# Kernel optimization log

Measured on AMD Instinct MI355X. Metric: run time of the kernel, lower is better.

The kernel has to match this reference:

```python
import jax, jax.numpy as jnp
import numpy as np

B, S, H = 16, 2048, 768
MAX_NUM = 400     # max relation pairs per sample (ragged, masked)
LABELS = 97
MID = 768


def setup_inputs() -> dict:
    key = jax.random.key(0)
    k1, k2, k3, k4, k5 = jax.random.split(key, 5)
    outs = jax.random.normal(k1, (B, S, H), dtype=jnp.float32)
    rels = jax.random.randint(k2, (B, MAX_NUM), 0, LABELS)
    start = jnp.ones((B,), dtype=jnp.int32)                     # markers start at pos 1
    num = jax.random.randint(k3, (B,), 1, MAX_NUM + 1)          # ragged counts in [1, MAX_NUM]
    rels_pos = jnp.stack([start, num], axis=1)                  # [B, 2]
    W1 = jax.random.normal(k4, (2 * H, MID), dtype=jnp.float32) * (1.0 / np.sqrt(2 * H))
    b1 = jnp.zeros((MID,), dtype=jnp.float32)
    W2 = jax.random.normal(k5, (MID, LABELS), dtype=jnp.float32) * (1.0 / np.sqrt(MID))
    b2 = jnp.zeros((LABELS,), dtype=jnp.float32)
    return {"outs": outs, "rels": rels, "rels_pos": rels_pos,
            "W1": W1, "b1": b1, "W2": W2, "b2": b2}


def reference(outs, rels, rels_pos, W1, b1, W2, b2):
    # outs: [B, S, H] encoder hidden states; rels_pos[:, 0]=start, [:, 1]=num (ragged)
    start = rels_pos[:, 0]          # [B]
    num = rels_pos[:, 1]            # [B]
    i = jnp.arange(MAX_NUM)         # [N]
    mask = i[None, :] < num[:, None]                 # [B, N] valid-pair mask
    pos1 = start[:, None] + 4 * i[None, :]           # head marker positions
    pos2 = pos1 + 2                                  # tail marker positions
    pos1 = jnp.clip(pos1, 0, S - 1)
    pos2 = jnp.clip(pos2, 0, S - 1)
    v1 = jnp.take_along_axis(outs, pos1[:, :, None], axis=1)   # [B, N, H]
    v2 = jnp.take_along_axis(outs, pos2[:, :, None], axis=1)   # [B, N, H]
    marker_vec = jnp.concatenate([v1, v2], axis=-1)             # [B, N, 2H]
    h = jax.nn.relu(jnp.einsum('bnd,dm->bnm', marker_vec, W1) + b1)
    logits = jnp.einsum('bnm,ml->bnl', h, W2) + b2              # [B, N, L]
    logp = jax.nn.log_softmax(logits, axis=-1)
    nll = -jnp.take_along_axis(logp, rels[:, :, None], axis=-1)[..., 0]  # [B, N]
    maskf = mask.astype(logits.dtype)
    loss = jnp.sum(nll * maskf) / jnp.sum(maskf)                # mean CE over valid pairs
    pred = jnp.where(mask, jnp.argmax(logits, axis=-1), -1)     # [B, N], -1 = padding
    label_vec = jnp.where(mask, rels, -1)
    return loss, pred, label_vec
```

## Files before the change

kernel.cpp:

```cpp
#include <hip/hip_runtime.h>
#include <hip/hip_bf16.h>
#include <math.h>

#define BB   16
#define SS   2048
#define HH   768
#define MAXN 400
#define LBL  97
#define MIDD 768
#define KTOT 1536

#define K2_XTILES 25
#define W1S_JOBS  (192 * 768)
#define K1_RT     7
#define K1_GROUPS (K1_RT * BB)
#define K1_BLOCKS (K1_GROUPS * 6)

typedef __attribute__((ext_vector_type(8)))  __bf16 bf16x8;
typedef __attribute__((ext_vector_type(16))) float  f32x16;

__global__ __launch_bounds__(256)
void k0_split(const float* __restrict__ W1, ushort* __restrict__ hi,
              ushort* __restrict__ lo)
{
    const int job = blockIdx.x * 256 + threadIdx.x;
    if (job >= W1S_JOBS) return;
    const int g   = job / 768;
    const int col = job - g * 768;
    bf16x8 hv, lv;
    #pragma unroll
    for (int j = 0; j < 8; ++j) {
        const float f = W1[(size_t)(g * 8 + j) * MIDD + col];
        const __bf16 hb = (__bf16)f;
        hv[j] = hb;
        lv[j] = (__bf16)(f - (float)hb);
    }
    ((bf16x8*)hi)[job] = hv;
    ((bf16x8*)lo)[job] = lv;
}

__global__ __launch_bounds__(256, 2)
void k1_gemm1(const float* __restrict__ outs, const int* __restrict__ rels_pos,
              const ushort* __restrict__ w1hi, const ushort* __restrict__ w1lo,
              const float* __restrict__ b1, float* __restrict__ h)
{
    const int gid = blockIdx.x;
    const int idx = gid >> 3;
    const int g   = (gid & 7) + 8 * (idx / 6);
    const int m   = idx % 6;
    const int rt  = g % K1_RT;
    const int b   = g / K1_RT;
    const int n0  = m * 128;
    const int i0  = rt * 64;

    const int num = rels_pos[2 * b + 1];
    if (i0 >= num) return;
    const int start = rels_pos[2 * b + 0];

    __shared__ __bf16 Ah[4][64][8];
    __shared__ __bf16 Al[4][64][8];
    __shared__ __bf16 Bh[4][128][8];
    __shared__ __bf16 Bl[4][128][8];

    const int tid = threadIdx.x;

    const int srow = tid & 63;
    const int sg   = tid >> 6;
    const int irow = i0 + srow;
    int p1 = start + 4 * irow;     p1 = min(max(p1, 0), SS - 1);
    int p2 = start + 4 * irow + 2; p2 = min(max(p2, 0), SS - 1);
    const float* arow1 = outs + (size_t)(b * SS + p1) * HH;
    const float* arow2 = outs + (size_t)(b * SS + p2) * HH;

    const int bc  = tid & 127;
    const int bg1 = tid >> 7;
    const int bg2 = 2 + (tid >> 7);
    const bf16x8* WH = (const bf16x8*)w1hi;
    const bf16x8* WL = (const bf16x8*)w1lo;

    const int lane = tid & 63;
    const int wid  = tid >> 6;
    const int wr   = wid >> 1;
    const int wc   = wid & 1;
    const int l31  = lane & 31;
    const int lhi  = lane >> 5;

    f32x16 acc[2];
    #pragma unroll
    for (int n = 0; n < 2; ++n)
        #pragma unroll
        for (int j = 0; j < 16; ++j) acc[n][j] = 0.f;

    float4 aU0, aV0, aU1, aV1;
    bf16x8 pB00, pB01, pB02, pB03, pB10, pB11, pB12, pB13;

    {
        const int k = sg * 8;
        const float* s = arow1 + k;
        aU0 = *(const float4*)(s);
        aV0 = *(const float4*)(s + 4);
        const size_t i1 = (size_t)bg1 * 768 + n0 + bc;
        const size_t i2 = (size_t)bg2 * 768 + n0 + bc;
        pB00 = WH[i1]; pB01 = WL[i1]; pB02 = WH[i2]; pB03 = WL[i2];
    }
    {
        const int k = 32 + sg * 8;
        const float* s = arow1 + k;
        aU1 = *(const float4*)(s);
        aV1 = *(const float4*)(s + 4);
        const size_t base = (size_t)(32 >> 3) * 768 + n0 + bc;
        const size_t i1 = base + (size_t)bg1 * 768;
        const size_t i2 = base + (size_t)bg2 * 768;
        pB10 = WH[i1]; pB11 = WL[i1]; pB12 = WH[i2]; pB13 = WL[i2];
    }

    #define K1_STAGE(AU, AV, P0, P1_, P2_, P3_)                               \
        {                                                                     \
            const float fa[8] = {AU.x, AU.y, AU.z, AU.w,                      \
                                 AV.x, AV.y, AV.z, AV.w};                     \
            bf16x8 ah, al;                                                    \
            _Pragma("unroll")                                                 \
            for (int j = 0; j < 8; ++j) {                                     \
                const __bf16 hb = (__bf16)fa[j];                              \
                ah[j] = hb;                                                   \
                al[j] = (__bf16)(fa[j] - (float)hb);                          \
            }                                                                 \
            *(bf16x8*)&Ah[sg][srow][0] = ah;                                  \
            *(bf16x8*)&Al[sg][srow][0] = al;                                  \
            *(bf16x8*)&Bh[bg1][bc][0]  = P0;                                  \
            *(bf16x8*)&Bl[bg1][bc][0]  = P1_;                                 \
            *(bf16x8*)&Bh[bg2][bc][0]  = P2_;                                 \
            *(bf16x8*)&Bl[bg2][bc][0]  = P3_;                                 \
        }

    #define K1_LOAD(AU, AV, P0, P1_, P2_, P3_, KT)                            \
        {                                                                     \
            const int k0 = (KT) * 32;                                         \
            const int k  = k0 + sg * 8;                                       \
            const float* s = (k < HH) ? (arow1 + k) : (arow2 + (k - HH));     \
            AU = *(const float4*)(s);                                         \
            AV = *(const float4*)(s + 4);                                     \
            const size_t base = (size_t)(k0 >> 3) * 768 + n0 + bc;            \
            const size_t i1 = base + (size_t)bg1 * 768;                       \
            const size_t i2 = base + (size_t)bg2 * 768;                       \
            P0 = WH[i1]; P1_ = WL[i1]; P2_ = WH[i2]; P3_ = WL[i2];            \
        }

    #define K1_MFMA()                                                         \
        _Pragma("unroll")                                                     \
        for (int s = 0; s < 2; ++s) {                                         \
            const int kg   = 2 * s + lhi;                                     \
            const int arow = wr * 32 + l31;                                   \
            const bf16x8 xh = *(const bf16x8*)&Ah[kg][arow][0];               \
            const bf16x8 xl = *(const bf16x8*)&Al[kg][arow][0];               \
            _Pragma("unroll")                                                 \
            for (int n = 0; n < 2; ++n) {                                     \
                const int bcol = wc * 64 + n * 32 + l31;                      \
                const bf16x8 yh = *(const bf16x8*)&Bh[kg][bcol][0];           \
                const bf16x8 yl = *(const bf16x8*)&Bl[kg][bcol][0];           \
                acc[n] = __builtin_amdgcn_mfma_f32_32x32x16_bf16(xh, yh, acc[n], 0, 0, 0); \
                acc[n] = __builtin_amdgcn_mfma_f32_32x32x16_bf16(xh, yl, acc[n], 0, 0, 0); \
                acc[n] = __builtin_amdgcn_mfma_f32_32x32x16_bf16(xl, yh, acc[n], 0, 0, 0); \
            }                                                                 \
        }

    for (int kt = 0; kt < KTOT / 32; kt += 2) {
        K1_STAGE(aU0, aV0, pB00, pB01, pB02, pB03);
        __syncthreads();
        if (kt + 2 < KTOT / 32) K1_LOAD(aU0, aV0, pB00, pB01, pB02, pB03, kt + 2);
        K1_MFMA();
        __syncthreads();
        K1_STAGE(aU1, aV1, pB10, pB11, pB12, pB13);
        __syncthreads();
        if (kt + 3 < KTOT / 32) K1_LOAD(aU1, aV1, pB10, pB11, pB12, pB13, kt + 3);
        K1_MFMA();
        __syncthreads();
    }
    #undef K1_STAGE
    #undef K1_LOAD
    #undef K1_MFMA

    #pragma unroll
    for (int n = 0; n < 2; ++n) {
        const int colg = n0 + wc * 64 + n * 32 + l31;
        const float bv = b1[colg];
        #pragma unroll
        for (int j = 0; j < 16; ++j) {
            const int row = (j & 3) + 8 * (j >> 2) + 4 * lhi;
            const int i = i0 + wr * 32 + row;
            if (i < MAXN)
                h[((size_t)b * MAXN + i) * MIDD + colg] = fmaxf(acc[n][j] + bv, 0.f);
        }
    }
}

__global__ __launch_bounds__(256, 2)
void k2_head(const float* __restrict__ h, const int* __restrict__ rels,
             const int* __restrict__ rels_pos,
             const float* __restrict__ W2, const float* __restrict__ b2,
             float* __restrict__ out, float* __restrict__ partials)
{
    const int b   = blockIdx.y;
    const int i0  = blockIdx.x * 16;
    const int num = rels_pos[2 * b + 1];
    const int tid = threadIdx.x;
    const int blk = blockIdx.y * gridDim.x + blockIdx.x;

    if (tid < 16) {
        const int i = i0 + tid;
        if (i < MAXN && i >= num) {
            out[1 + b * MAXN + i] = -1.0f;
            out[1 + BB * MAXN + b * MAXN + i] = -1.0f;
        }
    }
    if (i0 >= num) { if (tid == 0) partials[blk] = 0.f; return; }

    __shared__ __align__(16) float hs[MIDD][16];
    __shared__ float wave_nll[4];

    {
        const int row = tid & 15;
        const int kc0 = (tid >> 4) * 4;
        const int hrow_i = min(i0 + row, MAXN - 1);
        const float* hrow = h + ((size_t)b * MAXN + hrow_i) * MIDD;
        #pragma unroll
        for (int j = 0; j < 12; ++j) {
            const int k = kc0 + j * 64;
            const float4 v = *(const float4*)(hrow + k);
            hs[k + 0][row] = v.x;
            hs[k + 1][row] = v.y;
            hs[k + 2][row] = v.z;
            hs[k + 3][row] = v.w;
        }
    }
    __syncthreads();

    const int lane = tid & 63;
    const int wv   = tid >> 6;
    const int c    = lane;
    const bool has2 = (lane + 64) < LBL;
    const int c2   = has2 ? (lane + 64) : (LBL - 1);

    float acc0[4], acc1[4];
    #pragma unroll
    for (int r = 0; r < 4; ++r) { acc0[r] = 0.f; acc1[r] = 0.f; }

    float wA[8], wB[8], nAr[8], nBr[8];
    #pragma unroll
    for (int j = 0; j < 8; ++j) {
        wA[j] = W2[(size_t)j * LBL + c];
        wB[j] = W2[(size_t)j * LBL + c2];
    }
    for (int kbase = 0; kbase < MIDD; kbase += 8) {
        const bool more = (kbase + 8) < MIDD;
        if (more) {
            #pragma unroll
            for (int j = 0; j < 8; ++j) {
                nAr[j] = W2[(size_t)(kbase + 8 + j) * LBL + c];
                nBr[j] = W2[(size_t)(kbase + 8 + j) * LBL + c2];
            }
        }
        #pragma unroll
        for (int j = 0; j < 8; ++j) {
            const float4 hv = *(const float4*)&hs[kbase + j][wv * 4];
            acc0[0] += hv.x * wA[j]; acc0[1] += hv.y * wA[j];
            acc0[2] += hv.z * wA[j]; acc0[3] += hv.w * wA[j];
            acc1[0] += hv.x * wB[j]; acc1[1] += hv.y * wB[j];
            acc1[2] += hv.z * wB[j]; acc1[3] += hv.w * wB[j];
        }
        if (more) {
            #pragma unroll
            for (int j = 0; j < 8; ++j) { wA[j] = nAr[j]; wB[j] = nBr[j]; }
        }
    }
    const float bc  = b2[c];
    const float bc2 = b2[c2];
    #pragma unroll
    for (int r = 0; r < 4; ++r) { acc0[r] += bc; acc1[r] += bc2; }

    float nll_acc = 0.f;
    #pragma unroll
    for (int r = 0; r < 4; ++r) {
        const int i = i0 + wv * 4 + r;
        if (i >= num || i >= MAXN) continue;
        const float v1 = acc0[r];
        const float v2 = has2 ? acc1[r] : -INFINITY;
        float bv = v1; int bi = c;
        if (v2 > v1) { bv = v2; bi = lane + 64; }
        #pragma unroll
        for (int off = 32; off > 0; off >>= 1) {
            const float ov = __shfl_xor(bv, off);
            const int   oi = __shfl_xor(bi, off);
            if (ov > bv || (ov == bv && oi < bi)) { bv = ov; bi = oi; }
        }
        float se = expf(v1 - bv) + (has2 ? expf(v2 - bv) : 0.f);
        #pragma unroll
        for (int off = 32; off > 0; off >>= 1) se += __shfl_xor(se, off);
        const int lbl = rels[b * MAXN + i];
        float tv = (c == lbl ? v1 : 0.f) + ((has2 && (lane + 64) == lbl) ? v2 : 0.f);
        #pragma unroll
        for (int off = 32; off > 0; off >>= 1) tv += __shfl_xor(tv, off);
        const float nll = bv + logf(se) - tv;
        if (lane == 0) {
            nll_acc += nll;
            out[1 + b * MAXN + i] = (float)bi;
            out[1 + BB * MAXN + b * MAXN + i] = (float)lbl;
        }
    }
    if (lane == 0) wave_nll[wv] = nll_acc;
    __syncthreads();
    if (tid == 0)
        partials[blk] = wave_nll[0] + wave_nll[1] + wave_nll[2] + wave_nll[3];
}

__global__ void k3_final(const float* __restrict__ partials,
                         const int* __restrict__ rels_pos, float* __restrict__ out)
{
    const int lane = threadIdx.x;
    float v = 0.f;
    for (int idx = lane; idx < K2_XTILES * BB; idx += 64) v += partials[idx];
    #pragma unroll
    for (int off = 32; off > 0; off >>= 1) v += __shfl_xor(v, off);
    float cnt = (lane < BB) ? (float)min(max(rels_pos[2 * lane + 1], 0), MAXN) : 0.f;
    #pragma unroll
    for (int off = 32; off > 0; off >>= 1) cnt += __shfl_xor(cnt, off);
    if (lane == 0) out[0] = v / cnt;
}

extern "C" void kernel_launch(void* const* d_in, const int* in_sizes, int n_in,
                              void* d_out, int out_size, void* d_ws, size_t ws_size,
                              hipStream_t stream)
{
    const float* outs     = (const float*)d_in[0];
    const int*   rels     = (const int*)  d_in[1];
    const int*   rels_pos = (const int*)  d_in[2];
    const float* W1       = (const float*)d_in[3];
    const float* b1       = (const float*)d_in[4];
    const float* W2       = (const float*)d_in[5];
    const float* b2       = (const float*)d_in[6];
    float* out = (float*)d_out;

    float*  h        = (float*)d_ws;
    float*  partials = h + (size_t)BB * MAXN * MIDD;
    ushort* w1hi     = (ushort*)(partials + K2_XTILES * BB);
    ushort* w1lo     = w1hi + (size_t)W1S_JOBS * 8;

    hipLaunchKernelGGL(k0_split, dim3((W1S_JOBS + 255) / 256), dim3(256), 0, stream,
                       W1, w1hi, w1lo);

    hipLaunchKernelGGL(k1_gemm1, dim3(K1_BLOCKS), dim3(256), 0, stream,
                       outs, rels_pos, w1hi, w1lo, b1, h);

    dim3 g2(K2_XTILES, BB);
    hipLaunchKernelGGL(k2_head, g2, dim3(256), 0, stream,
                       h, rels, rels_pos, W2, b2, out, partials);

    hipLaunchKernelGGL(k3_final, dim3(1), dim3(64), 0, stream, partials, rels_pos, out);
}
```

Before: 287.3 us.

## Split GEMM1 K dimension four ways with atomic accumulation, move bias+ReLU to head

The first GEMM's K loop is split across four blocks per output tile, which multiplies the grid size so more CUs are busy on the ragged workload. Partial sums are combined with float atomicAdd into h, which is now zeroed with a memset beforehand. Bias and ReLU move into the head kernel's h load. In exchange it adds a 19.6 MB memset, atomic traffic on every h element, and results that depend on summation order.

```diff
diff --git a/kernel.cpp b/kernel.cpp
--- a/kernel.cpp
+++ b/kernel.cpp
@@ -14,7 +14,10 @@
 #define W1S_JOBS  (192 * 768)
 #define K1_RT     7
 #define K1_GROUPS (K1_RT * BB)
-#define K1_BLOCKS (K1_GROUPS * 6)
+#define K1_SPLIT  4
+#define K1_UNITS  (K1_GROUPS * K1_SPLIT)
+#define K1_BLOCKS (K1_UNITS * 6)
+#define K1_KI     (KTOT / 32 / K1_SPLIT)
 
 typedef __attribute__((ext_vector_type(8)))  __bf16 bf16x8;
 typedef __attribute__((ext_vector_type(16))) float  f32x16;
@@ -42,16 +45,19 @@
 __global__ __launch_bounds__(256, 2)
 void k1_gemm1(const float* __restrict__ outs, const int* __restrict__ rels_pos,
               const ushort* __restrict__ w1hi, const ushort* __restrict__ w1lo,
-              const float* __restrict__ b1, float* __restrict__ h)
+              float* __restrict__ h)
 {
     const int gid = blockIdx.x;
     const int idx = gid >> 3;
-    const int g   = (gid & 7) + 8 * (idx / 6);
+    const int u   = (gid & 7) + 8 * (idx / 6);
     const int m   = idx % 6;
+    const int g   = u >> 2;
+    const int s   = u & 3;
     const int rt  = g % K1_RT;
     const int b   = g / K1_RT;
     const int n0  = m * 128;
     const int i0  = rt * 64;
+    const int ks  = s * K1_KI;
 
     const int num = rels_pos[2 * b + 1];
     if (i0 >= num) return;
@@ -94,25 +100,18 @@
     float4 aU0, aV0, aU1, aV1;
     bf16x8 pB00, pB01, pB02, pB03, pB10, pB11, pB12, pB13;
 
-    {
-        const int k = sg * 8;
-        const float* s = arow1 + k;
-        aU0 = *(const float4*)(s);
-        aV0 = *(const float4*)(s + 4);
-        const size_t i1 = (size_t)bg1 * 768 + n0 + bc;
-        const size_t i2 = (size_t)bg2 * 768 + n0 + bc;
-        pB00 = WH[i1]; pB01 = WL[i1]; pB02 = WH[i2]; pB03 = WL[i2];
-    }
-    {
-        const int k = 32 + sg * 8;
-        const float* s = arow1 + k;
-        aU1 = *(const float4*)(s);
-        aV1 = *(const float4*)(s + 4);
-        const size_t base = (size_t)(32 >> 3) * 768 + n0 + bc;
-        const size_t i1 = base + (size_t)bg1 * 768;
-        const size_t i2 = base + (size_t)bg2 * 768;
-        pB10 = WH[i1]; pB11 = WL[i1]; pB12 = WH[i2]; pB13 = WL[i2];
-    }
+    #define K1_LOAD(AU, AV, P0, P1_, P2_, P3_, KT)                            \
+        {                                                                     \
+            const int k0 = (KT) * 32;                                         \
+            const int k  = k0 + sg * 8;                                       \
+            const float* sp = (k < HH) ? (arow1 + k) : (arow2 + (k - HH));    \
+            AU = *(const float4*)(sp);                                        \
+            AV = *(const float4*)(sp + 4);                                    \
+            const size_t base = (size_t)(k0 >> 3) * 768 + n0 + bc;            \
+            const size_t i1 = base + (size_t)bg1 * 768;                       \
+            const size_t i2 = base + (size_t)bg2 * 768;                       \
+            P0 = WH[i1]; P1_ = WL[i1]; P2_ = WH[i2]; P3_ = WL[i2];            \
+        }
 
     #define K1_STAGE(AU, AV, P0, P1_, P2_, P3_)                               \
         {                                                                     \
@@ -133,23 +132,10 @@
             *(bf16x8*)&Bl[bg2][bc][0]  = P3_;                                 \
         }
 
-    #define K1_LOAD(AU, AV, P0, P1_, P2_, P3_, KT)                            \
-        {                                                                     \
-            const int k0 = (KT) * 32;                                         \
-            const int k  = k0 + sg * 8;                                       \
-            const float* s = (k < HH) ? (arow1 + k) : (arow2 + (k - HH));     \
-            AU = *(const float4*)(s);                                         \
-            AV = *(const float4*)(s + 4);                                     \
-            const size_t base = (size_t)(k0 >> 3) * 768 + n0 + bc;            \
-            const size_t i1 = base + (size_t)bg1 * 768;                       \
-            const size_t i2 = base + (size_t)bg2 * 768;                       \
-            P0 = WH[i1]; P1_ = WL[i1]; P2_ = WH[i2]; P3_ = WL[i2];            \
-        }
-
     #define K1_MFMA()                                                         \
         _Pragma("unroll")                                                     \
-        for (int s = 0; s < 2; ++s) {                                         \
-            const int kg   = 2 * s + lhi;                                     \
+        for (int ss = 0; ss < 2; ++ss) {                                      \
+            const int kg   = 2 * ss + lhi;                                    \
             const int arow = wr * 32 + l31;                                   \
             const bf16x8 xh = *(const bf16x8*)&Ah[kg][arow][0];               \
             const bf16x8 xl = *(const bf16x8*)&Al[kg][arow][0];               \
@@ -164,15 +150,19 @@
             }                                                                 \
         }
 
-    for (int kt = 0; kt < KTOT / 32; kt += 2) {
+    K1_LOAD(aU0, aV0, pB00, pB01, pB02, pB03, ks);
+    K1_LOAD(aU1, aV1, pB10, pB11, pB12, pB13, ks + 1);
+
+    const int ke = ks + K1_KI;
+    for (int kt = ks; kt < ke; kt += 2) {
         K1_STAGE(aU0, aV0, pB00, pB01, pB02, pB03);
         __syncthreads();
-        if (kt + 2 < KTOT / 32) K1_LOAD(aU0, aV0, pB00, pB01, pB02, pB03, kt + 2);
+        if (kt + 2 < ke) K1_LOAD(aU0, aV0, pB00, pB01, pB02, pB03, kt + 2);
         K1_MFMA();
         __syncthreads();
         K1_STAGE(aU1, aV1, pB10, pB11, pB12, pB13);
         __syncthreads();
-        if (kt + 3 < KTOT / 32) K1_LOAD(aU1, aV1, pB10, pB11, pB12, pB13, kt + 3);
+        if (kt + 3 < ke) K1_LOAD(aU1, aV1, pB10, pB11, pB12, pB13, kt + 3);
         K1_MFMA();
         __syncthreads();
     }
@@ -183,20 +173,19 @@
     #pragma unroll
     for (int n = 0; n < 2; ++n) {
         const int colg = n0 + wc * 64 + n * 32 + l31;
-        const float bv = b1[colg];
         #pragma unroll
         for (int j = 0; j < 16; ++j) {
             const int row = (j & 3) + 8 * (j >> 2) + 4 * lhi;
             const int i = i0 + wr * 32 + row;
             if (i < MAXN)
-                h[((size_t)b * MAXN + i) * MIDD + colg] = fmaxf(acc[n][j] + bv, 0.f);
+                atomicAdd(&h[((size_t)b * MAXN + i) * MIDD + colg], acc[n][j]);
         }
     }
 }
 
 __global__ __launch_bounds__(256, 2)
-void k2_head(const float* __restrict__ h, const int* __restrict__ rels,
-             const int* __restrict__ rels_pos,
+void k2_head(const float* __restrict__ h, const float* __restrict__ b1,
+             const int* __restrict__ rels, const int* __restrict__ rels_pos,
              const float* __restrict__ W2, const float* __restrict__ b2,
              float* __restrict__ out, float* __restrict__ partials)
 {
@@ -226,11 +215,12 @@
         #pragma unroll
         for (int j = 0; j < 12; ++j) {
             const int k = kc0 + j * 64;
-            const float4 v = *(const float4*)(hrow + k);
-            hs[k + 0][row] = v.x;
-            hs[k + 1][row] = v.y;
-            hs[k + 2][row] = v.z;
-            hs[k + 3][row] = v.w;
+            const float4 v  = *(const float4*)(hrow + k);
+            const float4 bb = *(const float4*)(b1 + k);
+            hs[k + 0][row] = fmaxf(v.x + bb.x, 0.f);
+            hs[k + 1][row] = fmaxf(v.y + bb.y, 0.f);
+            hs[k + 2][row] = fmaxf(v.z + bb.z, 0.f);
+            hs[k + 3][row] = fmaxf(v.w + bb.w, 0.f);
         }
     }
     __syncthreads();
@@ -345,15 +335,17 @@
     ushort* w1hi     = (ushort*)(partials + K2_XTILES * BB);
     ushort* w1lo     = w1hi + (size_t)W1S_JOBS * 8;
 
+    hipMemsetAsync(h, 0, (size_t)BB * MAXN * MIDD * sizeof(float), stream);
+
     hipLaunchKernelGGL(k0_split, dim3((W1S_JOBS + 255) / 256), dim3(256), 0, stream,
                        W1, w1hi, w1lo);
 
     hipLaunchKernelGGL(k1_gemm1, dim3(K1_BLOCKS), dim3(256), 0, stream,
-                       outs, rels_pos, w1hi, w1lo, b1, h);
+                       outs, rels_pos, w1hi, w1lo, h);
 
     dim3 g2(K2_XTILES, BB);
     hipLaunchKernelGGL(k2_head, g2, dim3(256), 0, stream,
-                       h, rels, rels_pos, W2, b2, out, partials);
+                       h, b1, rels, rels_pos, W2, b2, out, partials);
 
     hipLaunchKernelGGL(k3_final, dim3(1), dim3(64), 0, stream, partials, rels_pos, out);
 }
```

Result: faster. 273.5 us (-4.8%).
